# Kernel tuning notes

Hardware: AMD Instinct MI355X
Metric: run time of the kernel (lower is better)

## Reference

```python
import jax, jax.numpy as jnp
import numpy as np

D_MODEL = 1024
N_HEADS = 16
D_HEAD = D_MODEL // N_HEADS

def setup_inputs() -> dict:
    key = jax.random.key(0)
    kx, kq, kk, kv, ko = jax.random.split(key, 5)
    s = 1.0 / np.sqrt(D_MODEL)
    return {
        "x": jax.random.normal(kx, (4, 2048, D_MODEL), dtype=jnp.float32),
        "W_q": jax.random.normal(kq, (D_MODEL, D_MODEL), dtype=jnp.float32) * s,
        "W_k": jax.random.normal(kk, (D_MODEL, D_MODEL), dtype=jnp.float32) * s,
        "W_v": jax.random.normal(kv, (D_MODEL, D_MODEL), dtype=jnp.float32) * s,
        "W_o": jax.random.normal(ko, (D_MODEL, D_MODEL), dtype=jnp.float32) * s,
    }

def reference(x, W_q, W_k, W_v, W_o):
    B, L, _ = x.shape
    def heads(h):  # (B,L,D) -> (B,H,L,d_head)
        return h.reshape(B, L, N_HEADS, D_HEAD).transpose(0, 2, 1, 3)
    # nn.Linear: y = x @ W.T
    q = heads(x @ W_q.T)
    k = heads(x @ W_k.T)
    v = heads(x @ W_v.T)
    scores = jnp.einsum('bhqd,bhkd->bhqk', q, k) / jnp.sqrt(jnp.float32(D_HEAD))
    attn = jax.nn.softmax(scores, axis=-1)
    ctx = jnp.einsum('bhqk,bhkd->bhqd', attn, v)
    ctx = ctx.transpose(0, 2, 1, 3).reshape(B, L, D_MODEL)
    return ctx @ W_o.T
```

## Files before the change

kernel.cpp:

```cpp
#include <hip/hip_runtime.h>
#include <hip/hip_fp16.h>

typedef _Float16 f16;
typedef _Float16 f16x2 __attribute__((ext_vector_type(2)));
typedef _Float16 f16x4 __attribute__((ext_vector_type(4)));
typedef _Float16 f16x8 __attribute__((ext_vector_type(8)));
typedef float f32x4 __attribute__((ext_vector_type(4)));
typedef float f32x16 __attribute__((ext_vector_type(16)));

#define NHEADS 16
#define DHEAD 64
#define DM 1024
#define BATCH 4
#define SEQ 2048
#define MTOT (BATCH*SEQ)

__device__ inline void gload_lds16(const void* g, void* l) {
  __builtin_amdgcn_global_load_lds(
      (const __attribute__((address_space(1))) void*)g,
      (__attribute__((address_space(3))) void*)l, 16, 0, 0);
}

__device__ inline float max3f(float a, float b, float c) {
  return fmaxf(fmaxf(a, b), c);
}

__device__ inline unsigned pkrtz(float a, float b) {
  auto h = __builtin_amdgcn_cvt_pkrtz(a, b);
  unsigned u; __builtin_memcpy(&u, &h, 4); return u;
}

__device__ inline float xmax32(float x) { return fmaxf(x, __shfl_xor(x, 32)); }
__device__ inline float xsum32(float x) { return x + __shfl_xor(x, 32); }

__device__ inline float accum2(unsigned w, float acc) {
  f16x2 p; __builtin_memcpy(&p, &w, 4);
#if __has_builtin(__builtin_amdgcn_fdot2)
  const f16x2 one2 = {(f16)1, (f16)1};
  return __builtin_amdgcn_fdot2(p, one2, acc, false);
#else
  return acc + (float)p[0] + (float)p[1];
#endif
}

__global__ __launch_bounds__(256) void cvt_f32_f16_k(const float* __restrict__ s,
                                                     f16* __restrict__ d, int n) {
  int i = (blockIdx.x * 256 + threadIdx.x) * 8;
  if (i + 8 <= n) {
    float4 a = *reinterpret_cast<const float4*>(s + i);
    float4 b = *reinterpret_cast<const float4*>(s + i + 4);
    f16x8 h = {(f16)a.x,(f16)a.y,(f16)a.z,(f16)a.w,(f16)b.x,(f16)b.y,(f16)b.z,(f16)b.w};
    *reinterpret_cast<f16x8*>(d + i) = h;
  } else {
    for (int j = i; j < n; ++j) d[j] = (f16)s[j];
  }
}

__global__ __launch_bounds__(256) void cvt_w4_k(const float* __restrict__ w0,
                                                const float* __restrict__ w1,
                                                const float* __restrict__ w2,
                                                const float* __restrict__ w3,
                                                f16* __restrict__ d) {
  int which = blockIdx.x >> 9;
  const float* s = which == 0 ? w0 : which == 1 ? w1 : which == 2 ? w2 : w3;
  int off = ((blockIdx.x & 511) * 256 + threadIdx.x) * 8;
  float4 a = *reinterpret_cast<const float4*>(s + off);
  float4 b = *reinterpret_cast<const float4*>(s + off + 4);
  f16x8 h = {(f16)a.x,(f16)a.y,(f16)a.z,(f16)a.w,(f16)b.x,(f16)b.y,(f16)b.z,(f16)b.w};
  *reinterpret_cast<f16x8*>(d + (size_t)which * DM * DM + off) = h;
}

template <int MODE>
__device__ void gemm_nt_body(const f16* __restrict__ A, const f16* __restrict__ Bw,
                             void* __restrict__ outp, int m0, int n0, float oscale,
                             f16* Ah, f16* Bh) {
  const int tx = threadIdx.x;
  const int wave = tx >> 6, lane = tx & 63;
  const int wm = (wave >> 1) * 64, wn = (wave & 1) * 64;

  f32x4 acc[4][4];
#pragma unroll
  for (int i = 0; i < 4; ++i)
#pragma unroll
    for (int j = 0; j < 4; ++j) acc[i][j] = {0.f, 0.f, 0.f, 0.f};

  const int srow = lane >> 2;
  const int scol = (lane & 3) * 8;

  auto stage = [&](int buf, int k0) {
#pragma unroll
    for (int i = 0; i < 2; ++i) {
      int chunk = wave * 2 + i;
      gload_lds16(A  + (size_t)(m0 + chunk * 16 + srow) * DM + k0 + scol,
                  Ah + buf * 4096 + chunk * 512);
      gload_lds16(Bw + (size_t)(n0 + chunk * 16 + srow) * DM + k0 + scol,
                  Bh + buf * 4096 + chunk * 512);
    }
  };

  stage(0, 0);
  __syncthreads();
  for (int k0 = 0; k0 < DM; k0 += 32) {
    const int cur = (k0 >> 5) & 1;
    if (k0 + 32 < DM) stage(cur ^ 1, k0 + 32);

    const f16* Ac = Ah + cur * 4096;
    const f16* Bc = Bh + cur * 4096;
    f16x8 af[4], bf[4];
#pragma unroll
    for (int i = 0; i < 4; ++i)
      af[i] = *reinterpret_cast<const f16x8*>(Ac + (wm + i * 16 + (lane & 15)) * 32 + (lane >> 4) * 8);
#pragma unroll
    for (int j = 0; j < 4; ++j)
      bf[j] = *reinterpret_cast<const f16x8*>(Bc + (wn + j * 16 + (lane & 15)) * 32 + (lane >> 4) * 8);
#pragma unroll
    for (int i = 0; i < 4; ++i)
#pragma unroll
      for (int j = 0; j < 4; ++j)
        acc[i][j] = __builtin_amdgcn_mfma_f32_16x16x32_f16(af[i], bf[j], acc[i][j], 0, 0, 0);
    __syncthreads();
  }

  const int r0 = (lane >> 4) * 4, c0 = lane & 15;
#pragma unroll
  for (int i = 0; i < 4; ++i)
#pragma unroll
    for (int j = 0; j < 4; ++j)
#pragma unroll
      for (int r = 0; r < 4; ++r) {
        int gm = m0 + wm + i * 16 + r0 + r;
        int gn = n0 + wn + j * 16 + c0;
        float v = acc[i][j][r] * oscale;
        if (MODE == 2) {
          ((float*)outp)[(size_t)gm * DM + gn] = v;
        } else {
          int b = gm >> 11, l = gm & 2047, h = gn >> 6, d = gn & 63;
          size_t idx = (MODE == 0)
            ? (((size_t)(b * NHEADS + h) * SEQ + l) * DHEAD + d)
            : (((size_t)(b * NHEADS + h) * DHEAD + d) * SEQ + l);
          ((f16*)outp)[idx] = (f16)v;
        }
      }
}

__global__ __launch_bounds__(256) void gemm_qkv(const f16* __restrict__ xh,
                                                const f16* __restrict__ Wf,
                                                f16* __restrict__ Qb,
                                                f16* __restrict__ Kb,
                                                f16* __restrict__ VTb,
                                                float qscale) {
  __shared__ f16 Ah[2 * 128 * 32];
  __shared__ f16 Bh[2 * 128 * 32];
  const int m0 = blockIdx.x * 128;
  const int cc = blockIdx.y;
  const int which = cc >> 3;
  const int n0 = (cc & 7) * 128;
  const f16* Bw = Wf + (size_t)which * DM * DM;
  if (which == 0)      gemm_nt_body<0>(xh, Bw, Qb,  m0, n0, qscale, Ah, Bh);
  else if (which == 1) gemm_nt_body<0>(xh, Bw, Kb,  m0, n0, 1.0f,  Ah, Bh);
  else                 gemm_nt_body<1>(xh, Bw, VTb, m0, n0, 1.0f,  Ah, Bh);
}

__global__ __launch_bounds__(256) void gemm_out(const f16* __restrict__ A,
                                                const f16* __restrict__ Bw,
                                                float* __restrict__ outp) {
  __shared__ f16 Ah[2 * 128 * 32];
  __shared__ f16 Bh[2 * 128 * 32];
  gemm_nt_body<2>(A, Bw, outp, blockIdx.x * 128, blockIdx.y * 128, 1.0f, Ah, Bh);
}

__global__ __launch_bounds__(512, 4) void attn_k(const f16* __restrict__ Q,
                                                 const f16* __restrict__ Kg,
                                                 const f16* __restrict__ VT,
                                                 f16* __restrict__ ctx) {
  __shared__ f16 Kt[2][128 * 64];
  __shared__ f16 Vt[2][64 * 128];
  const int tx = threadIdx.x, wave = tx >> 6, lane = tx & 63;
  const int m = lane & 31, hi = lane >> 5, m7 = m & 7;

  const int bid = blockIdx.y * 8 + blockIdx.x;
  const int swz = (bid & 7) * 64 + (bid >> 3);
  const int bh = swz >> 3;
  const int q0 = (swz & 7) * 256;

  const f16* Qb = Q  + (size_t)bh * SEQ * DHEAD;
  const f16* Kb = Kg + (size_t)bh * SEQ * DHEAD;
  const f16* Vb = VT + (size_t)bh * DHEAD * SEQ;

  const int rk = tx >> 3;
  const int sk = ((tx & 7) ^ (rk & 7)) * 8;
  const int rv = tx >> 4;
  const int sv = ((tx & 15) ^ (rv & 7)) * 8;

  auto stage = [&](int buf, int k0) {
    gload_lds16(Kb + (size_t)(k0 + rk) * DHEAD + sk,      &Kt[buf][(size_t)(wave * 64) * 8]);
    gload_lds16(Kb + (size_t)(k0 + 64 + rk) * DHEAD + sk, &Kt[buf][(size_t)(512 + wave * 64) * 8]);
    gload_lds16(Vb + (size_t)rv * SEQ + k0 + sv,          &Vt[buf][(size_t)(wave * 64) * 8]);
    gload_lds16(Vb + (size_t)(32 + rv) * SEQ + k0 + sv,   &Vt[buf][(size_t)(512 + wave * 64) * 8]);
  };

  f16x8 qb[4];
#pragma unroll
  for (int s = 0; s < 4; ++s)
    qb[s] = *reinterpret_cast<const f16x8*>(
        Qb + (size_t)(q0 + wave * 32 + m) * DHEAD + s * 16 + hi * 8);

  f32x16 oacc[2];
#pragma unroll
  for (int r = 0; r < 16; ++r) { oacc[0][r] = 0.f; oacc[1][r] = 0.f; }
  float lsum = 0.f;
  float mrun = -1e30f;

  auto compute = [&](const f16* Kc, const f16* Vc) {
#pragma unroll
    for (int kt = 0; kt < 4; ++kt) {
      f32x16 st;
#pragma unroll
      for (int r = 0; r < 16; ++r) st[r] = 0.f;
      __builtin_amdgcn_s_setprio(1);
#pragma unroll
      for (int s = 0; s < 4; ++s) {
        f16x8 ka = *reinterpret_cast<const f16x8*>(
            Kc + ((kt * 32 + m) * 8 + ((2 * s + hi) ^ m7)) * 8);
        st = __builtin_amdgcn_mfma_f32_32x32x16_f16(ka, qb[s], st, 0, 0, 0);
      }
      __builtin_amdgcn_s_setprio(0);

      float a0 = max3f(st[0], st[1], st[2]);
      float a1 = max3f(st[3], st[4], st[5]);
      float a2 = max3f(st[6], st[7], st[8]);
      float a3 = max3f(st[9], st[10], st[11]);
      float a4 = max3f(st[12], st[13], st[14]);
      float mx = fmaxf(fmaxf(max3f(a0, a1, a2), fmaxf(a3, a4)), st[15]);
      mx = xmax32(mx);

      if (!__all(mx <= mrun + 8.f)) {
        float mnew = fmaxf(mrun, mx);
        float scl = __builtin_amdgcn_exp2f(mrun - mnew);
#pragma unroll
        for (int r = 0; r < 16; ++r) { oacc[0][r] *= scl; oacc[1][r] *= scl; }
        lsum *= scl;
        mrun = mnew;
      }

      unsigned pk[8];
#pragma unroll
      for (int j = 0; j < 8; ++j)
        pk[j] = pkrtz(__builtin_amdgcn_exp2f(st[2 * j] - mrun),
                      __builtin_amdgcn_exp2f(st[2 * j + 1] - mrun));
#pragma unroll
      for (int j = 0; j < 8; ++j) lsum = accum2(pk[j], lsum);

      __builtin_amdgcn_s_setprio(1);
#pragma unroll
      for (int c1 = 0; c1 < 2; ++c1) {
        const int c = kt * 2 + c1;
        unsigned w0 = pk[4 * c1 + 0], w1 = pk[4 * c1 + 1];
        unsigned w2 = pk[4 * c1 + 2], w3 = pk[4 * c1 + 3];
        asm("v_permlane32_swap_b32 %0, %1" : "+v"(w0), "+v"(w2));
        asm("v_permlane32_swap_b32 %0, %1" : "+v"(w1), "+v"(w3));
        union { unsigned u[4]; f16x8 h; } pu;
        pu.u[0] = w0; pu.u[1] = w1; pu.u[2] = w2; pu.u[3] = w3;
#pragma unroll
        for (int dt = 0; dt < 2; ++dt) {
          f16x8 va = *reinterpret_cast<const f16x8*>(
              Vc + ((dt * 32 + m) * 16 + ((2 * c + hi) ^ m7)) * 8);
          oacc[dt] = __builtin_amdgcn_mfma_f32_32x32x16_f16(va, pu.h, oacc[dt], 0, 0, 0);
        }
      }
      __builtin_amdgcn_s_setprio(0);
    }
  };

  stage(0, 0);
  __syncthreads();
  for (int tt = 0; tt < 16; tt += 2) {
    stage(1, (tt + 1) * 128);
    compute(Kt[0], Vt[0]);
    __syncthreads();
    if (tt + 2 < 16) stage(0, (tt + 2) * 128);
    compute(Kt[1], Vt[1]);
    __syncthreads();
  }

  const float ltot = xsum32(lsum);
  const float inv = 1.0f / ltot;
  const int b = bh >> 4, hd = bh & 15;
  const int q = q0 + wave * 32 + m;
  f16* obase = ctx + ((size_t)b * SEQ + q) * DM + hd * DHEAD;
#pragma unroll
  for (int dt = 0; dt < 2; ++dt)
#pragma unroll
    for (int t = 0; t < 4; ++t) {
      f16x4 o = {(f16)(oacc[dt][4 * t + 0] * inv), (f16)(oacc[dt][4 * t + 1] * inv),
                 (f16)(oacc[dt][4 * t + 2] * inv), (f16)(oacc[dt][4 * t + 3] * inv)};
      *reinterpret_cast<f16x4*>(obase + dt * 32 + t * 8 + 4 * hi) = o;
    }
}

extern "C" void kernel_launch(void* const* d_in, const int* in_sizes, int n_in,
                              void* d_out, int out_size, void* d_ws, size_t ws_size,
                              hipStream_t stream) {
  (void)in_sizes; (void)n_in; (void)out_size; (void)ws_size;
  const float* x  = (const float*)d_in[0];
  const float* Wq = (const float*)d_in[1];
  const float* Wk = (const float*)d_in[2];
  const float* Wv = (const float*)d_in[3];
  const float* Wo = (const float*)d_in[4];

  char* ws = (char*)d_ws;
  const size_t SZ_X = (size_t)MTOT * DM * sizeof(f16);
  const size_t SZ_W = (size_t)DM * DM * sizeof(f16);
  f16* xh  = (f16*)(ws);
  f16* wfh = (f16*)(ws + SZ_X);
  f16* woh = (f16*)(ws + SZ_X + 3 * SZ_W);
  f16* Qb  = (f16*)(ws + 1 * SZ_X + 4 * SZ_W);
  f16* Kb  = (f16*)(ws + 2 * SZ_X + 4 * SZ_W);
  f16* VTb = (f16*)(ws + 3 * SZ_X + 4 * SZ_W);
  f16* ctx = xh;

  const int nx = MTOT * DM;
  const float QSCALE = 0.125f * 1.44269504088896f;

  cvt_f32_f16_k<<<nx / 2048, 256, 0, stream>>>(x, xh, nx);
  cvt_w4_k<<<2048, 256, 0, stream>>>(Wq, Wk, Wv, Wo, wfh);

  gemm_qkv<<<dim3(64, 24), 256, 0, stream>>>(xh, wfh, Qb, Kb, VTb, QSCALE);

  attn_k<<<dim3(SEQ / 256, BATCH * NHEADS), 512, 0, stream>>>(Qb, Kb, VTb, ctx);

  gemm_out<<<dim3(64, 8), 256, 0, stream>>>(ctx, woh, (float*)d_out);
}
```

Before: 219.4 us.

## Triple-buffer GEMM LDS staging with explicit vmcnt waits and reorder grid

The shared GEMM body moves from double to triple buffering of LDS tiles, prefetching two k-steps ahead. It uses an explicit s_waitcnt vmcnt plus raw s_barrier in place of __syncthreads, so global-to-LDS loads overlap the MFMA work. The grid for both GEMMs is also transposed so that consecutive blocks share the same A row tile across N tiles, which should improve L2 reuse of activations. The cost is more LDS per block, which may lower occupancy, and the hand-written waitcnt counts must be correct for the pipeline to stay safe.

```diff
diff --git a/kernel.cpp b/kernel.cpp
--- a/kernel.cpp
+++ b/kernel.cpp
@@ -99,10 +99,20 @@
   };
 
   stage(0, 0);
-  __syncthreads();
-  for (int k0 = 0; k0 < DM; k0 += 32) {
-    const int cur = (k0 >> 5) & 1;
-    if (k0 + 32 < DM) stage(cur ^ 1, k0 + 32);
+  stage(1, 32);
+  int cur = 0, nxt = 2;
+  for (int t = 0; t < 32; ++t) {
+    if (t < 31) {
+      asm volatile("s_waitcnt vmcnt(4)" ::: "memory");
+    } else {
+      asm volatile("s_waitcnt vmcnt(0)" ::: "memory");
+    }
+    __builtin_amdgcn_sched_barrier(0);
+    __builtin_amdgcn_s_barrier();
+    if (t + 2 < 32) {
+      stage(nxt, (t + 2) * 32);
+      nxt = nxt == 2 ? 0 : nxt + 1;
+    }
 
     const f16* Ac = Ah + cur * 4096;
     const f16* Bc = Bh + cur * 4096;
@@ -118,7 +128,8 @@
 #pragma unroll
       for (int j = 0; j < 4; ++j)
         acc[i][j] = __builtin_amdgcn_mfma_f32_16x16x32_f16(af[i], bf[j], acc[i][j], 0, 0, 0);
-    __syncthreads();
+    __builtin_amdgcn_s_barrier();
+    cur = cur == 2 ? 0 : cur + 1;
   }
 
   const int r0 = (lane >> 4) * 4, c0 = lane & 15;
@@ -149,12 +160,11 @@
                                                 f16* __restrict__ Kb,
                                                 f16* __restrict__ VTb,
                                                 float qscale) {
-  __shared__ f16 Ah[2 * 128 * 32];
-  __shared__ f16 Bh[2 * 128 * 32];
-  const int m0 = blockIdx.x * 128;
-  const int cc = blockIdx.y;
-  const int which = cc >> 3;
-  const int n0 = (cc & 7) * 128;
+  __shared__ f16 Ah[3 * 4096];
+  __shared__ f16 Bh[3 * 4096];
+  const int which = blockIdx.x >> 3;
+  const int n0 = (blockIdx.x & 7) * 128;
+  const int m0 = blockIdx.y * 128;
   const f16* Bw = Wf + (size_t)which * DM * DM;
   if (which == 0)      gemm_nt_body<0>(xh, Bw, Qb,  m0, n0, qscale, Ah, Bh);
   else if (which == 1) gemm_nt_body<0>(xh, Bw, Kb,  m0, n0, 1.0f,  Ah, Bh);
@@ -164,9 +174,9 @@
 __global__ __launch_bounds__(256) void gemm_out(const f16* __restrict__ A,
                                                 const f16* __restrict__ Bw,
                                                 float* __restrict__ outp) {
-  __shared__ f16 Ah[2 * 128 * 32];
-  __shared__ f16 Bh[2 * 128 * 32];
-  gemm_nt_body<2>(A, Bw, outp, blockIdx.x * 128, blockIdx.y * 128, 1.0f, Ah, Bh);
+  __shared__ f16 Ah[3 * 4096];
+  __shared__ f16 Bh[3 * 4096];
+  gemm_nt_body<2>(A, Bw, outp, blockIdx.y * 128, blockIdx.x * 128, 1.0f, Ah, Bh);
 }
 
 __global__ __launch_bounds__(512, 4) void attn_k(const f16* __restrict__ Q,
@@ -325,9 +335,9 @@
   cvt_f32_f16_k<<<nx / 2048, 256, 0, stream>>>(x, xh, nx);
   cvt_w4_k<<<2048, 256, 0, stream>>>(Wq, Wk, Wv, Wo, wfh);
 
-  gemm_qkv<<<dim3(64, 24), 256, 0, stream>>>(xh, wfh, Qb, Kb, VTb, QSCALE);
+  gemm_qkv<<<dim3(24, MTOT / 128), 256, 0, stream>>>(xh, wfh, Qb, Kb, VTb, QSCALE);
 
   attn_k<<<dim3(SEQ / 256, BATCH * NHEADS), 512, 0, stream>>>(Qb, Kb, VTb, ctx);
 
-  gemm_out<<<dim3(64, 8), 256, 0, stream>>>(ctx, woh, (float*)d_out);
-}
+  gemm_out<<<dim3(DM / 128, MTOT / 128), 256, 0, stream>>>(ctx, woh, (float*)d_out);
+}
```

After: 229.9 us. +4.8%, slower.
